# Kernel tuning notes

Hardware: AMD Instinct MI355X
Metric: run time of the kernel (lower is better)

Reference implementation:

```python
import jax, jax.numpy as jnp
import numpy as np


def setup_inputs() -> dict:
    key = jax.random.key(0)
    kA, kB = jax.random.split(key)
    B, H, W, C = 1, 80, 80, 256  # NHWC backbone features; B must be 1 for the TF broadcast in the divide to be valid
    feature_A = jax.random.normal(kA, (B, H, W, C), dtype=jnp.float32)
    feature_B = jax.random.normal(kB, (B, H, W, C), dtype=jnp.float32)
    return {"feature_A": feature_A, "feature_B": feature_B}


def reference(feature_A, feature_B):
    # corr[b,i,j,k,l] = mean_c A[b,i,j,c] * B[b,k,l,c]
    # Expressed as a batched matmul instead of materializing the (H,W,H,W,C) intermediate.
    C = feature_A.shape[-1]
    corr = jnp.einsum('bijc,bklc->bijkl', feature_A, feature_B) / C  # [B,H,W,H,W]
    # penalty[b,i,j] = sqrt(sum_{k,l} corr^2)
    penalty = jnp.sqrt(jnp.sum(corr * corr, axis=(-1, -2)))  # [B,H,W]
    # Faithful to tf.math.divide: trailing-dim broadcasting of [B,H,W] against [B,H,W,H,W]
    # (valid because B == 1; penalty aligns to the (j,k,l) trailing axes exactly as in TF).
    return corr / penalty
```

## Files before the change

kernel.cpp:

```cpp
#include <hip/hip_runtime.h>

typedef __attribute__((ext_vector_type(8))) short bf16x8;
typedef __attribute__((ext_vector_type(4))) float f32x4;

#define M_TOT 6400
#define C_TOT 256
#define BM 128
#define BN 128
#define BK 32
#define NTILE 50
#define ONM 50
#define ONN 25

#define VMCNT0 asm volatile("s_waitcnt vmcnt(0)" ::: "memory")
#define VMCNT4 asm volatile("s_waitcnt vmcnt(4)" ::: "memory")
#define VMCNT6 asm volatile("s_waitcnt vmcnt(6)" ::: "memory")
#define SBAR   __builtin_amdgcn_s_barrier()

__device__ __forceinline__ short f2bf(float f) {
    unsigned u = __float_as_uint(f);
    u = (u + 0x7fffu + ((u >> 16) & 1u)) >> 16;
    return (short)u;
}
__device__ __forceinline__ float bf2f(short s) {
    return __uint_as_float(((unsigned)(unsigned short)s) << 16);
}

__device__ __forceinline__ void gload16(const short* g, short* l) {
    __builtin_amdgcn_global_load_lds(
        (const __attribute__((address_space(1))) void*)g,
        (__attribute__((address_space(3))) void*)l, 16, 0, 0);
}


__global__ __launch_bounds__(256) void prep(const float* __restrict__ A,
                                            const float* __restrict__ Bm,
                                            short* __restrict__ Ab,
                                            short* __restrict__ Bb,
                                            short* __restrict__ Bt,
                                            float* __restrict__ P)
{
    __shared__ __align__(16) short Lb[64][72];
    const int bid = blockIdx.x;
    const int t   = threadIdx.x;

    if (bid < 400) {
        const int n0 = (bid % 100) * 64;
        const int c0 = (bid / 100) * 64;
        const int r  = t >> 2;
        const int cb = (t & 3) * 16;

        const float4* src = reinterpret_cast<const float4*>(
            Bm + (size_t)(n0 + r) * C_TOT + c0 + cb);
        const float4 v0 = src[0], v1 = src[1], v2 = src[2], v3 = src[3];
        bf16x8 w0, w1;
        w0[0]=f2bf(v0.x); w0[1]=f2bf(v0.y); w0[2]=f2bf(v0.z); w0[3]=f2bf(v0.w);
        w0[4]=f2bf(v1.x); w0[5]=f2bf(v1.y); w0[6]=f2bf(v1.z); w0[7]=f2bf(v1.w);
        w1[0]=f2bf(v2.x); w1[1]=f2bf(v2.y); w1[2]=f2bf(v2.z); w1[3]=f2bf(v2.w);
        w1[4]=f2bf(v3.x); w1[5]=f2bf(v3.y); w1[6]=f2bf(v3.z); w1[7]=f2bf(v3.w);
        *reinterpret_cast<bf16x8*>(&Lb[r][cb])     = w0;
        *reinterpret_cast<bf16x8*>(&Lb[r][cb + 8]) = w1;
        short* brow = Bb + (size_t)(n0 + r) * C_TOT + c0 + cb;
        *reinterpret_cast<bf16x8*>(brow)     = w0;
        *reinterpret_cast<bf16x8*>(brow + 8) = w1;
        __syncthreads();

        #pragma unroll
        for (int p = 0; p < 2; ++p) {
            const int q = t + p * 256;
            const int c = q >> 3;
            const int h = q & 7;
            bf16x8 w;
            #pragma unroll
            for (int j = 0; j < 8; ++j) w[j] = Lb[h * 8 + j][c];
            *reinterpret_cast<bf16x8*>(&Bt[(size_t)(c0 + c) * M_TOT + n0 + h * 8]) = w;
        }
    } else {
        const int aid = bid - 400;
        if (aid == 0)
            for (int j = t; j < M_TOT; j += 256) P[j] = 0.0f;
        const int base = aid * 2048;
        #pragma unroll
        for (int it = 0; it < 8; ++it) {
            const int i = base + it * 256 + t;
            const float4 v0 = reinterpret_cast<const float4*>(A + (size_t)i * 8)[0];
            const float4 v1 = reinterpret_cast<const float4*>(A + (size_t)i * 8)[1];
            bf16x8 w;
            w[0]=f2bf(v0.x); w[1]=f2bf(v0.y); w[2]=f2bf(v0.z); w[3]=f2bf(v0.w);
            w[4]=f2bf(v1.x); w[5]=f2bf(v1.y); w[6]=f2bf(v1.z); w[7]=f2bf(v1.w);
            *reinterpret_cast<bf16x8*>(Ab + (size_t)i * 8) = w;
        }
    }
}

__global__ __launch_bounds__(256) void convert_ab(const float* __restrict__ A,
                                                  const float* __restrict__ Bm,
                                                  short* __restrict__ Ab,
                                                  short* __restrict__ Bb)
{
    const int n8 = M_TOT * C_TOT / 8;
    for (int i = blockIdx.x * blockDim.x + threadIdx.x; i < 2 * n8;
         i += gridDim.x * blockDim.x) {
        const float* s = (i < n8) ? (A + (size_t)i * 8) : (Bm + (size_t)(i - n8) * 8);
        short* d       = (i < n8) ? (Ab + (size_t)i * 8) : (Bb + (size_t)(i - n8) * 8);
        const float4 v0 = reinterpret_cast<const float4*>(s)[0];
        const float4 v1 = reinterpret_cast<const float4*>(s)[1];
        bf16x8 w;
        w[0]=f2bf(v0.x); w[1]=f2bf(v0.y); w[2]=f2bf(v0.z); w[3]=f2bf(v0.w);
        w[4]=f2bf(v1.x); w[5]=f2bf(v1.y); w[6]=f2bf(v1.z); w[7]=f2bf(v1.w);
        *reinterpret_cast<bf16x8*>(d) = w;
    }
}


__device__ __forceinline__ void stage_tiles_g(const short* __restrict__ A,
                                              const short* __restrict__ B,
                                              int m0, int n0, int k0,
                                              int lda, int ldb,
                                              short* As, short* Bs,
                                              int wave, int lane)
{
    #pragma unroll
    for (int t = 0; t < 2; ++t) {
        const int c  = (wave * 2 + t) * 64 + lane;
        const int r  = c >> 2;
        const int g  = c & 3;
        const int sg = g ^ ((r >> 1) & 3);
        gload16(A + (size_t)(m0 + r) * lda + k0 + sg * 8, As + (wave * 2 + t) * 512);
        gload16(B + (size_t)(n0 + r) * ldb + k0 + sg * 8, Bs + (wave * 2 + t) * 512);
    }
}

template<int KSTEPS>
__device__ __forceinline__ void gemm_tile_g(const short* __restrict__ A,
                                            const short* __restrict__ B,
                                            int m0, int n0, int kbase,
                                            int lda, int ldb, int tid,
                                            short (*Sm)[2][4096],
                                            f32x4 acc[4][4])
{
    const int lane = tid & 63;
    const int wave = tid >> 6;
    const int rl   = lane & 15;
    const int g_rd = lane >> 4;
    const int wr   = wave >> 1;
    const int wc   = wave & 1;

    stage_tiles_g(A, B, m0, n0, kbase, lda, ldb, &Sm[0][0][0], &Sm[0][1][0], wave, lane);
    if (KSTEPS > 1)
        stage_tiles_g(A, B, m0, n0, kbase + BK, lda, ldb,
                      &Sm[1][0][0], &Sm[1][1][0], wave, lane);
    if (KSTEPS > 1) { VMCNT4; } else { VMCNT0; }
    SBAR;

    #pragma unroll
    for (int kt = 0; kt < KSTEPS; ++kt) {
        const int cur = kt % 3;
        if (kt + 2 < KSTEPS)
            stage_tiles_g(A, B, m0, n0, kbase + (kt + 2) * BK, lda, ldb,
                          &Sm[(kt + 2) % 3][0][0], &Sm[(kt + 2) % 3][1][0], wave, lane);

        bf16x8 af[4], bfr[4];
        #pragma unroll
        for (int mi = 0; mi < 4; ++mi) {
            const int r  = wr * 64 + mi * 16 + rl;
            const int sg = g_rd ^ ((r >> 1) & 3);
            af[mi] = *reinterpret_cast<const bf16x8*>(&Sm[cur][0][r * BK + sg * 8]);
        }
        #pragma unroll
        for (int ni = 0; ni < 4; ++ni) {
            const int r  = wc * 64 + ni * 16 + rl;
            const int sg = g_rd ^ ((r >> 1) & 3);
            bfr[ni] = *reinterpret_cast<const bf16x8*>(&Sm[cur][1][r * BK + sg * 8]);
        }
        __builtin_amdgcn_s_setprio(1);
        #pragma unroll
        for (int mi = 0; mi < 4; ++mi)
            #pragma unroll
            for (int ni = 0; ni < 4; ++ni)
                acc[mi][ni] = __builtin_amdgcn_mfma_f32_16x16x32_bf16(
                    af[mi], bfr[ni], acc[mi][ni], 0, 0, 0);
        __builtin_amdgcn_s_setprio(0);

        if (kt + 1 < KSTEPS) {
            if (kt + 2 < KSTEPS) { VMCNT4; } else { VMCNT0; }
            SBAR;
        }
    }
}


template<int STEPS>
__global__ __launch_bounds__(256) void gemm_G(const short* __restrict__ Bt,
                                              float* __restrict__ Gp)
{
    __shared__ __align__(16) short Sm[3][2][4096];
    const int tid = threadIdx.x;
    const int m0 = blockIdx.y * BM, n0 = blockIdx.x * BN;
    const int z  = blockIdx.z;
    f32x4 acc[4][4] = {};
    gemm_tile_g<STEPS>(Bt, Bt, m0, n0, z * (STEPS * BK),
                       M_TOT, M_TOT, tid, Sm, acc);

    float* dst = Gp + (size_t)z * (C_TOT * C_TOT);
    const int lane = tid & 63, rl = lane & 15;
    const int wave = tid >> 6, wr = wave >> 1, wc = wave & 1;
    #pragma unroll
    for (int mi = 0; mi < 4; ++mi)
        #pragma unroll
        for (int i = 0; i < 4; ++i) {
            const int m = m0 + wr * 64 + mi * 16 + (lane >> 4) * 4 + i;
            #pragma unroll
            for (int ni = 0; ni < 4; ++ni)
                dst[m * C_TOT + n0 + wc * 64 + ni * 16 + rl] = acc[mi][ni][i];
        }
}

__global__ __launch_bounds__(256) void g_reduce(const float* __restrict__ Gp,
                                                short* __restrict__ Gb,
                                                int nchunks)
{
    const int i4 = blockIdx.x * 256 + threadIdx.x;
    float4 s = make_float4(0.f, 0.f, 0.f, 0.f);
    for (int z = 0; z < nchunks; ++z) {
        const float4 v = reinterpret_cast<const float4*>(
            Gp + (size_t)z * (C_TOT * C_TOT))[i4];
        s.x += v.x; s.y += v.y; s.z += v.z; s.w += v.w;
    }
    short4 o;
    o.x = f2bf(s.x); o.y = f2bf(s.y); o.z = f2bf(s.z); o.w = f2bf(s.w);
    reinterpret_cast<short4*>(Gb)[i4] = o;
}

__global__ __launch_bounds__(256) void penalty_q(const short* __restrict__ Ab,
                                                 const short* __restrict__ Gb,
                                                 float* __restrict__ P)
{
    __shared__ __align__(16) short Sm[3][2][4096];
    const int tid = threadIdx.x;
    const int m0 = blockIdx.x * BM;
    const int ci = blockIdx.y & 1, cj = blockIdx.y >> 1;
    const int lane = tid & 63, rl = lane & 15;
    const int wave = tid >> 6, wr = wave >> 1, wc = wave & 1;

    f32x4 acc[4][4] = {};
    gemm_tile_g<4>(Ab, Gb + (size_t)(cj * BM) * C_TOT, m0, 0, ci * BM,
                   C_TOT, C_TOT, tid, Sm, acc);

    #pragma unroll
    for (int mi = 0; mi < 4; ++mi)
        #pragma unroll
        for (int i = 0; i < 4; ++i) {
            const int m = m0 + wr * 64 + mi * 16 + (lane >> 4) * 4 + i;
            float s = 0.0f;
            #pragma unroll
            for (int ni = 0; ni < 4; ++ni) {
                const int cp = cj * BM + wc * 64 + ni * 16 + rl;
                s += acc[mi][ni][i] * bf2f(Ab[(size_t)m * C_TOT + cp]);
            }
            s += __shfl_xor(s, 1);
            s += __shfl_xor(s, 2);
            s += __shfl_xor(s, 4);
            s += __shfl_xor(s, 8);
            if (rl == 0) atomicAdd(&P[m], s);
        }
}


#define OBUF 12288
#define OB_B 4096

__device__ __forceinline__ void stage_tiles_o(const short* __restrict__ A,
                                              const short* __restrict__ B,
                                              int m0, int n0, int k0,
                                              short* buf, int wave, int lane)
{
    #pragma unroll
    for (int t = 0; t < 2; ++t) {
        const int c  = (wave * 2 + t) * 64 + lane;
        const int r  = c >> 2;
        const int g  = c & 3;
        const int sg = g ^ ((r >> 1) & 3);
        gload16(A + (size_t)(m0 + r) * C_TOT + k0 + sg * 8, buf + (wave * 2 + t) * 512);
    }
    #pragma unroll
    for (int t = 0; t < 4; ++t) {
        const int c  = (wave * 4 + t) * 64 + lane;
        const int r  = c >> 2;
        const int g  = c & 3;
        const int sg = g ^ ((r >> 1) & 3);
        gload16(B + (size_t)(n0 + r) * C_TOT + k0 + sg * 8,
                buf + OB_B + (wave * 4 + t) * 512);
    }
}

__global__ __launch_bounds__(256, 2) void gemm_out(const short* __restrict__ Ab,
                                                   const short* __restrict__ Bb,
                                                   const float* __restrict__ P,
                                                   float* __restrict__ out)
{
    __shared__ __align__(16) short Sm[3][OBUF];
    const int tid = threadIdx.x;
    const int lane = tid & 63, rl = lane & 15;
    const int g_rd = lane >> 4;
    const int wave = tid >> 6, wr = wave >> 1, wc = wave & 1;

    const int nwg = ONM * ONN, q = nwg >> 3, r = nwg & 7;
    const int orig = blockIdx.x;
    const int xcd = orig & 7, idx = orig >> 3;
    const int wg = (xcd < r ? xcd * (q + 1) : r * (q + 1) + (xcd - r) * q) + idx;
    const int m0 = (wg / ONN) * 128;
    const int n0 = (wg % ONN) * 256;

    f32x4 acc[4][8] = {};

    stage_tiles_o(Ab, Bb, m0, n0, 0,  &Sm[0][0], wave, lane);
    stage_tiles_o(Ab, Bb, m0, n0, BK, &Sm[1][0], wave, lane);
    VMCNT6; SBAR;

    #pragma unroll
    for (int kt = 0; kt < 8; ++kt) {
        const int cur = kt % 3;
        if (kt + 2 < 8)
            stage_tiles_o(Ab, Bb, m0, n0, (kt + 2) * BK, &Sm[(kt + 2) % 3][0], wave, lane);

        bf16x8 af[4], bfr[8];
        #pragma unroll
        for (int mi = 0; mi < 4; ++mi) {
            const int rr = wr * 64 + mi * 16 + rl;
            const int sg = g_rd ^ ((rr >> 1) & 3);
            af[mi] = *reinterpret_cast<const bf16x8*>(&Sm[cur][rr * BK + sg * 8]);
        }
        #pragma unroll
        for (int ni = 0; ni < 8; ++ni) {
            const int rr = wc * 128 + ni * 16 + rl;
            const int sg = g_rd ^ ((rr >> 1) & 3);
            bfr[ni] = *reinterpret_cast<const bf16x8*>(&Sm[cur][OB_B + rr * BK + sg * 8]);
        }
        __builtin_amdgcn_s_setprio(1);
        #pragma unroll
        for (int mi = 0; mi < 4; ++mi)
            #pragma unroll
            for (int ni = 0; ni < 8; ++ni)
                acc[mi][ni] = __builtin_amdgcn_mfma_f32_16x16x32_bf16(
                    af[mi], bfr[ni], acc[mi][ni], 0, 0, 0);
        __builtin_amdgcn_s_setprio(0);

        if (kt + 1 < 8) {
            if (kt + 2 < 8) { VMCNT6; } else { VMCNT0; }
            SBAR;
        }
    }

    float rs[8];
    #pragma unroll
    for (int ni = 0; ni < 8; ++ni)
        rs[ni] = rsqrtf(P[n0 + wc * 128 + ni * 16 + rl]);

    SBAR;

    float* Es = reinterpret_cast<float*>(Sm) + wave * 2112;
    #pragma unroll
    for (int mi = 0; mi < 4; ++mi) {
        #pragma unroll
        for (int ni = 0; ni < 8; ++ni)
            #pragma unroll
            for (int i = 0; i < 4; ++i)
                Es[((lane >> 4) * 4 + i) * 132 + ni * 16 + rl] = acc[mi][ni][i] * rs[ni];
        #pragma unroll
        for (int it = 0; it < 8; ++it) {
            const int f   = it * 64 + lane;
            const int row = f >> 5;
            const int c4  = f & 31;
            const float4 v = *reinterpret_cast<const float4*>(&Es[row * 132 + c4 * 4]);
            const int m = m0 + wr * 64 + mi * 16 + row;
            *reinterpret_cast<float4*>(
                &out[(size_t)m * M_TOT + n0 + wc * 128 + c4 * 4]) = v;
        }
    }
}


__global__ __launch_bounds__(256) void gemm_penalty(const short* __restrict__ Ab,
                                                    const short* __restrict__ Bb,
                                                    float* __restrict__ P)
{
    __shared__ __align__(16) short Sm[3][2][4096];
    const int tid = threadIdx.x;
    const int m0 = blockIdx.y * BM, n0 = blockIdx.x * BN;
    f32x4 acc[4][4] = {};
    gemm_tile_g<8>(Ab, Bb, m0, n0, 0, C_TOT, C_TOT, tid, Sm, acc);

    const int lane = tid & 63, rl = lane & 15;
    const int wave = tid >> 6, wr = wave >> 1;
    #pragma unroll
    for (int mi = 0; mi < 4; ++mi) {
        #pragma unroll
        for (int i = 0; i < 4; ++i) {
            const int m = m0 + wr * 64 + mi * 16 + (lane >> 4) * 4 + i;
            float s = 0.0f;
            #pragma unroll
            for (int ni = 0; ni < 4; ++ni) {
                const float v = acc[mi][ni][i];
                s += v * v;
            }
            s += __shfl_xor(s, 1);
            s += __shfl_xor(s, 2);
            s += __shfl_xor(s, 4);
            s += __shfl_xor(s, 8);
            if (rl == 0) atomicAdd(&P[m], s);
        }
    }
}

__global__ __launch_bounds__(256) void gemm_out_plain(const short* __restrict__ Ab,
                                                      const short* __restrict__ Bb,
                                                      const float* __restrict__ P,
                                                      float* __restrict__ out)
{
    __shared__ __align__(16) short Sm[3][2][4096];
    const int tid = threadIdx.x;
    const int lane = tid & 63, rl = lane & 15;
    const int wave = tid >> 6, wr = wave >> 1, wc = wave & 1;
    const int m0 = blockIdx.y * BM, n0 = blockIdx.x * BN;

    f32x4 acc[4][4] = {};
    gemm_tile_g<8>(Ab, Bb, m0, n0, 0, C_TOT, C_TOT, tid, Sm, acc);

    float rs[4];
    #pragma unroll
    for (int ni = 0; ni < 4; ++ni)
        rs[ni] = rsqrtf(P[n0 + wc * 64 + ni * 16 + rl]);

    SBAR;

    float* Es = reinterpret_cast<float*>(Sm) + wave * 1088;
    #pragma unroll
    for (int mi = 0; mi < 4; ++mi) {
        #pragma unroll
        for (int ni = 0; ni < 4; ++ni)
            #pragma unroll
            for (int i = 0; i < 4; ++i)
                Es[((lane >> 4) * 4 + i) * 68 + ni * 16 + rl] = acc[mi][ni][i] * rs[ni];
        #pragma unroll
        for (int it = 0; it < 4; ++it) {
            const int f   = it * 64 + lane;
            const int row = f >> 4;
            const int c4  = f & 15;
            const float4 v = *reinterpret_cast<const float4*>(&Es[row * 68 + c4 * 4]);
            const int m = m0 + wr * 64 + mi * 16 + row;
            *reinterpret_cast<float4*>(&out[(size_t)m * M_TOT + n0 + wc * 64 + c4 * 4]) = v;
        }
    }
}


__global__ __launch_bounds__(256) void corr_gemm(const float* __restrict__ A,
                                                 const float* __restrict__ Bm,
                                                 float* __restrict__ out,
                                                 float* __restrict__ penalty)
{
    __shared__ short As[BM * BK];
    __shared__ short Bs[BN * BK];

    const int tid  = threadIdx.x;
    const int lane = tid & 63;
    const int wave = tid >> 6;
    const int wr   = wave >> 1;
    const int wc   = wave & 1;
    const int m0   = blockIdx.y * BM;
    const int n0   = blockIdx.x * BN;
    const int g_rd = lane >> 4;
    const int rl   = lane & 15;

    f32x4 acc[4][4] = {};

    for (int k0 = 0; k0 < C_TOT; k0 += BK) {
        #pragma unroll
        for (int half = 0; half < 2; ++half) {
            const int cc = tid + half * 256;
            const int r  = cc >> 2;
            const int g  = cc & 3;
            const int sg = g ^ ((r >> 1) & 3);

            const float4* pa = reinterpret_cast<const float4*>(
                A + (size_t)(m0 + r) * C_TOT + k0 + g * 8);
            float4 a0 = pa[0], a1 = pa[1];
            bf16x8 wa;
            wa[0]=f2bf(a0.x); wa[1]=f2bf(a0.y); wa[2]=f2bf(a0.z); wa[3]=f2bf(a0.w);
            wa[4]=f2bf(a1.x); wa[5]=f2bf(a1.y); wa[6]=f2bf(a1.z); wa[7]=f2bf(a1.w);
            *reinterpret_cast<bf16x8*>(&As[r * BK + sg * 8]) = wa;

            const float4* pb = reinterpret_cast<const float4*>(
                Bm + (size_t)(n0 + r) * C_TOT + k0 + g * 8);
            float4 b0 = pb[0], b1 = pb[1];
            bf16x8 wb;
            wb[0]=f2bf(b0.x); wb[1]=f2bf(b0.y); wb[2]=f2bf(b0.z); wb[3]=f2bf(b0.w);
            wb[4]=f2bf(b1.x); wb[5]=f2bf(b1.y); wb[6]=f2bf(b1.z); wb[7]=f2bf(b1.w);
            *reinterpret_cast<bf16x8*>(&Bs[r * BK + sg * 8]) = wb;
        }
        __syncthreads();

        bf16x8 af[4], bfr[4];
        #pragma unroll
        for (int mi = 0; mi < 4; ++mi) {
            const int r  = wr * 64 + mi * 16 + rl;
            const int sg = g_rd ^ ((r >> 1) & 3);
            af[mi] = *reinterpret_cast<const bf16x8*>(&As[r * BK + sg * 8]);
        }
        #pragma unroll
        for (int ni = 0; ni < 4; ++ni) {
            const int r  = wc * 64 + ni * 16 + rl;
            const int sg = g_rd ^ ((r >> 1) & 3);
            bfr[ni] = *reinterpret_cast<const bf16x8*>(&Bs[r * BK + sg * 8]);
        }
        #pragma unroll
        for (int mi = 0; mi < 4; ++mi)
            #pragma unroll
            for (int ni = 0; ni < 4; ++ni)
                acc[mi][ni] = __builtin_amdgcn_mfma_f32_16x16x32_bf16(
                    af[mi], bfr[ni], acc[mi][ni], 0, 0, 0);
        __syncthreads();
    }

    const float inv_c = 1.0f / (float)C_TOT;
    #pragma unroll
    for (int mi = 0; mi < 4; ++mi) {
        #pragma unroll
        for (int i = 0; i < 4; ++i) {
            const int m = m0 + wr * 64 + mi * 16 + (lane >> 4) * 4 + i;
            float s = 0.0f;
            #pragma unroll
            for (int ni = 0; ni < 4; ++ni) {
                const float v = acc[mi][ni][i] * inv_c;
                out[(size_t)m * M_TOT + n0 + wc * 64 + ni * 16 + rl] = v;
                s += v * v;
            }
            s += __shfl_xor(s, 1);
            s += __shfl_xor(s, 2);
            s += __shfl_xor(s, 4);
            s += __shfl_xor(s, 8);
            if (rl == 0) atomicAdd(&penalty[m], s);
        }
    }
}

__global__ __launch_bounds__(256) void scale_k(float* __restrict__ out,
                                               const float* __restrict__ penalty)
{
    const unsigned cols4 = M_TOT / 4;
    const unsigned total = (unsigned)M_TOT * cols4;
    float4* o4 = reinterpret_cast<float4*>(out);
    const float4* p4 = reinterpret_cast<const float4*>(penalty);
    for (unsigned idx = blockIdx.x * blockDim.x + threadIdx.x; idx < total;
         idx += gridDim.x * blockDim.x) {
        const unsigned n4 = idx % cols4;
        const float4 p = p4[n4];
        float4 v = o4[idx];
        v.x *= rsqrtf(p.x);
        v.y *= rsqrtf(p.y);
        v.z *= rsqrtf(p.z);
        v.w *= rsqrtf(p.w);
        o4[idx] = v;
    }
}


extern "C" void kernel_launch(void* const* d_in, const int* in_sizes, int n_in,
                              void* d_out, int out_size, void* d_ws, size_t ws_size,
                              hipStream_t stream) {
    const float* A = (const float*)d_in[0];
    const float* B = (const float*)d_in[1];
    float* out     = (float*)d_out;

    const size_t mat_sh = (size_t)M_TOT * C_TOT;
    const size_t sz_ab  = mat_sh * sizeof(short);
    const size_t sz_gb  = (size_t)C_TOT * C_TOT * sizeof(short);
    const size_t sz_p   = (size_t)M_TOT * sizeof(float);
    const size_t sz_gq  = (size_t)C_TOT * C_TOT * sizeof(float);
    const size_t base_need = 3 * sz_ab + sz_gb + sz_p;
    const size_t need_f40  = base_need + 40 * sz_gq;
    const size_t need_f20  = base_need + 20 * sz_gq;
    const size_t need_mid  = 2 * sz_ab + sz_p;

    dim3 grid2(NTILE, NTILE);

    if (ws_size >= need_f20) {
        short* Ab = (short*)d_ws;
        short* Bb = Ab + mat_sh;
        short* Bt = Bb + mat_sh;
        short* Gb = Bt + mat_sh;
        float* P  = (float*)((char*)d_ws + 3 * sz_ab + sz_gb);
        float* Gp = (float*)((char*)d_ws + 3 * sz_ab + sz_gb + sz_p);

        prep<<<500, 256, 0, stream>>>(A, B, Ab, Bb, Bt, P);
        if (ws_size >= need_f40) {
            gemm_G<5><<<dim3(2, 2, 40), 256, 0, stream>>>(Bt, Gp);
            g_reduce<<<64, 256, 0, stream>>>(Gp, Gb, 40);
        } else {
            gemm_G<10><<<dim3(2, 2, 20), 256, 0, stream>>>(Bt, Gp);
            g_reduce<<<64, 256, 0, stream>>>(Gp, Gb, 20);
        }
        penalty_q<<<dim3(NTILE, 4), 256, 0, stream>>>(Ab, Gb, P);
        gemm_out<<<ONM * ONN, 256, 0, stream>>>(Ab, Bb, P, out);
    } else if (ws_size >= need_mid) {
        short* Ab = (short*)d_ws;
        short* Bb = Ab + mat_sh;
        float* P  = (float*)(Bb + mat_sh);

        hipMemsetAsync(P, 0, sz_p, stream);
        convert_ab<<<1600, 256, 0, stream>>>(A, B, Ab, Bb);
        gemm_penalty<<<grid2, dim3(256), 0, stream>>>(Ab, Bb, P);
        gemm_out_plain<<<grid2, dim3(256), 0, stream>>>(Ab, Bb, P, out);
    } else {
        float* penalty = (float*)d_ws;
        hipMemsetAsync(penalty, 0, sz_p, stream);
        corr_gemm<<<grid2, dim3(256), 0, stream>>>(A, B, out, penalty);
        scale_k<<<2048, 256, 0, stream>>>(out, penalty);
    }
}
```

Baseline: 84.01 us.

## Split gemm_out across 8 waves with 64x64 per-wave tiles and nontemporal stores

The output GEMM kernel moves from 256 threads (4 waves, each computing 64x128) to 512 threads (8 waves, each computing 64x64) for the same 128x256 block tile. Global-to-LDS staging is spread over more waves and the vmcnt waits are adjusted to match. Final output writes now use nontemporal stores so the large streamed output bypasses cache retention. This cuts per-wave accumulator registers and raises wave count per CU to hide latency, in exchange for more LDS fragment reads per MFMA and more barrier participants.

```diff
diff --git a/kernel.cpp b/kernel.cpp
--- a/kernel.cpp
+++ b/kernel.cpp
@@ -13,8 +13,8 @@
 #define ONN 25
 
 #define VMCNT0 asm volatile("s_waitcnt vmcnt(0)" ::: "memory")
+#define VMCNT3 asm volatile("s_waitcnt vmcnt(3)" ::: "memory")
 #define VMCNT4 asm volatile("s_waitcnt vmcnt(4)" ::: "memory")
-#define VMCNT6 asm volatile("s_waitcnt vmcnt(6)" ::: "memory")
 #define SBAR   __builtin_amdgcn_s_barrier()
 
 __device__ __forceinline__ short f2bf(float f) {
@@ -93,6 +93,276 @@
     }
 }
 
+
+__device__ __forceinline__ void stage_tiles_g(const short* __restrict__ A,
+                                              const short* __restrict__ B,
+                                              int m0, int n0, int k0,
+                                              int lda, int ldb,
+                                              short* As, short* Bs,
+                                              int wave, int lane)
+{
+    #pragma unroll
+    for (int t = 0; t < 2; ++t) {
+        const int c  = (wave * 2 + t) * 64 + lane;
+        const int r  = c >> 2;
+        const int g  = c & 3;
+        const int sg = g ^ ((r >> 1) & 3);
+        gload16(A + (size_t)(m0 + r) * lda + k0 + sg * 8, As + (wave * 2 + t) * 512);
+        gload16(B + (size_t)(n0 + r) * ldb + k0 + sg * 8, Bs + (wave * 2 + t) * 512);
+    }
+}
+
+template<int KSTEPS>
+__device__ __forceinline__ void gemm_tile_g(const short* __restrict__ A,
+                                            const short* __restrict__ B,
+                                            int m0, int n0, int kbase,
+                                            int lda, int ldb, int tid,
+                                            short (*Sm)[2][4096],
+                                            f32x4 acc[4][4])
+{
+    const int lane = tid & 63;
+    const int wave = tid >> 6;
+    const int rl   = lane & 15;
+    const int g_rd = lane >> 4;
+    const int wr   = wave >> 1;
+    const int wc   = wave & 1;
+
+    stage_tiles_g(A, B, m0, n0, kbase, lda, ldb, &Sm[0][0][0], &Sm[0][1][0], wave, lane);
+    if (KSTEPS > 1)
+        stage_tiles_g(A, B, m0, n0, kbase + BK, lda, ldb,
+                      &Sm[1][0][0], &Sm[1][1][0], wave, lane);
+    if (KSTEPS > 1) { VMCNT4; } else { VMCNT0; }
+    SBAR;
+
+    #pragma unroll
+    for (int kt = 0; kt < KSTEPS; ++kt) {
+        const int cur = kt % 3;
+        if (kt + 2 < KSTEPS)
+            stage_tiles_g(A, B, m0, n0, kbase + (kt + 2) * BK, lda, ldb,
+                          &Sm[(kt + 2) % 3][0][0], &Sm[(kt + 2) % 3][1][0], wave, lane);
+
+        bf16x8 af[4], bfr[4];
+        #pragma unroll
+        for (int mi = 0; mi < 4; ++mi) {
+            const int r  = wr * 64 + mi * 16 + rl;
+            const int sg = g_rd ^ ((r >> 1) & 3);
+            af[mi] = *reinterpret_cast<const bf16x8*>(&Sm[cur][0][r * BK + sg * 8]);
+        }
+        #pragma unroll
+        for (int ni = 0; ni < 4; ++ni) {
+            const int r  = wc * 64 + ni * 16 + rl;
+            const int sg = g_rd ^ ((r >> 1) & 3);
+            bfr[ni] = *reinterpret_cast<const bf16x8*>(&Sm[cur][1][r * BK + sg * 8]);
+        }
+        __builtin_amdgcn_s_setprio(1);
+        #pragma unroll
+        for (int mi = 0; mi < 4; ++mi)
+            #pragma unroll
+            for (int ni = 0; ni < 4; ++ni)
+                acc[mi][ni] = __builtin_amdgcn_mfma_f32_16x16x32_bf16(
+                    af[mi], bfr[ni], acc[mi][ni], 0, 0, 0);
+        __builtin_amdgcn_s_setprio(0);
+
+        if (kt + 1 < KSTEPS) {
+            if (kt + 2 < KSTEPS) { VMCNT4; } else { VMCNT0; }
+            SBAR;
+        }
+    }
+}
+
+
+template<int STEPS>
+__global__ __launch_bounds__(256) void gemm_G(const short* __restrict__ Bt,
+                                              float* __restrict__ Gp)
+{
+    __shared__ __align__(16) short Sm[3][2][4096];
+    const int tid = threadIdx.x;
+    const int m0 = blockIdx.y * BM, n0 = blockIdx.x * BN;
+    const int z  = blockIdx.z;
+    f32x4 acc[4][4] = {};
+    gemm_tile_g<STEPS>(Bt, Bt, m0, n0, z * (STEPS * BK),
+                       M_TOT, M_TOT, tid, Sm, acc);
+
+    float* dst = Gp + (size_t)z * (C_TOT * C_TOT);
+    const int lane = tid & 63, rl = lane & 15;
+    const int wave = tid >> 6, wr = wave >> 1, wc = wave & 1;
+    #pragma unroll
+    for (int mi = 0; mi < 4; ++mi)
+        #pragma unroll
+        for (int i = 0; i < 4; ++i) {
+            const int m = m0 + wr * 64 + mi * 16 + (lane >> 4) * 4 + i;
+            #pragma unroll
+            for (int ni = 0; ni < 4; ++ni)
+                dst[m * C_TOT + n0 + wc * 64 + ni * 16 + rl] = acc[mi][ni][i];
+        }
+}
+
+__global__ __launch_bounds__(256) void g_reduce(const float* __restrict__ Gp,
+                                                short* __restrict__ Gb,
+                                                int nchunks)
+{
+    const int i4 = blockIdx.x * 256 + threadIdx.x;
+    float4 s = make_float4(0.f, 0.f, 0.f, 0.f);
+    for (int z = 0; z < nchunks; ++z) {
+        const float4 v = reinterpret_cast<const float4*>(
+            Gp + (size_t)z * (C_TOT * C_TOT))[i4];
+        s.x += v.x; s.y += v.y; s.z += v.z; s.w += v.w;
+    }
+    short4 o;
+    o.x = f2bf(s.x); o.y = f2bf(s.y); o.z = f2bf(s.z); o.w = f2bf(s.w);
+    reinterpret_cast<short4*>(Gb)[i4] = o;
+}
+
+__global__ __launch_bounds__(256) void penalty_q(const short* __restrict__ Ab,
+                                                 const short* __restrict__ Gb,
+                                                 float* __restrict__ P)
+{
+    __shared__ __align__(16) short Sm[3][2][4096];
+    const int tid = threadIdx.x;
+    const int m0 = blockIdx.x * BM;
+    const int ci = blockIdx.y & 1, cj = blockIdx.y >> 1;
+    const int lane = tid & 63, rl = lane & 15;
+    const int wave = tid >> 6, wr = wave >> 1, wc = wave & 1;
+
+    f32x4 acc[4][4] = {};
+    gemm_tile_g<4>(Ab, Gb + (size_t)(cj * BM) * C_TOT, m0, 0, ci * BM,
+                   C_TOT, C_TOT, tid, Sm, acc);
+
+    #pragma unroll
+    for (int mi = 0; mi < 4; ++mi)
+        #pragma unroll
+        for (int i = 0; i < 4; ++i) {
+            const int m = m0 + wr * 64 + mi * 16 + (lane >> 4) * 4 + i;
+            float s = 0.0f;
+            #pragma unroll
+            for (int ni = 0; ni < 4; ++ni) {
+                const int cp = cj * BM + wc * 64 + ni * 16 + rl;
+                s += acc[mi][ni][i] * bf2f(Ab[(size_t)m * C_TOT + cp]);
+            }
+            s += __shfl_xor(s, 1);
+            s += __shfl_xor(s, 2);
+            s += __shfl_xor(s, 4);
+            s += __shfl_xor(s, 8);
+            if (rl == 0) atomicAdd(&P[m], s);
+        }
+}
+
+
+#define OBUF 12288
+#define OB_B 4096
+
+__device__ __forceinline__ void stage_512(const short* __restrict__ A,
+                                          const short* __restrict__ B,
+                                          int m0, int n0, int k0,
+                                          short* buf, int wave, int lane)
+{
+    {
+        const int c  = wave * 64 + lane;
+        const int r  = c >> 2;
+        const int g  = c & 3;
+        const int sg = g ^ ((r >> 1) & 3);
+        gload16(A + (size_t)(m0 + r) * C_TOT + k0 + sg * 8, buf + wave * 512);
+    }
+    #pragma unroll
+    for (int tt = 0; tt < 2; ++tt) {
+        const int c  = (wave * 2 + tt) * 64 + lane;
+        const int r  = c >> 2;
+        const int g  = c & 3;
+        const int sg = g ^ ((r >> 1) & 3);
+        gload16(B + (size_t)(n0 + r) * C_TOT + k0 + sg * 8,
+                buf + OB_B + (wave * 2 + tt) * 512);
+    }
+}
+
+__global__ __launch_bounds__(512, 4) void gemm_out(const short* __restrict__ Ab,
+                                                   const short* __restrict__ Bb,
+                                                   const float* __restrict__ P,
+                                                   float* __restrict__ out)
+{
+    __shared__ __align__(16) short Sm[3][OBUF];
+    const int tid = threadIdx.x;
+    const int lane = tid & 63, rl = lane & 15;
+    const int g_rd = lane >> 4;
+    const int wave = tid >> 6;
+    const int wr   = wave >> 2;
+    const int wc   = wave & 3;
+
+    const int nwg = ONM * ONN, q = nwg >> 3, r = nwg & 7;
+    const int orig = blockIdx.x;
+    const int xcd = orig & 7, idx = orig >> 3;
+    const int wg = (xcd < r ? xcd * (q + 1) : r * (q + 1) + (xcd - r) * q) + idx;
+    const int m0 = (wg / ONN) * 128;
+    const int n0 = (wg % ONN) * 256;
+
+    f32x4 acc[4][4] = {};
+
+    stage_512(Ab, Bb, m0, n0, 0,  &Sm[0][0], wave, lane);
+    stage_512(Ab, Bb, m0, n0, BK, &Sm[1][0], wave, lane);
+    VMCNT3; SBAR;
+
+    #pragma unroll
+    for (int kt = 0; kt < 8; ++kt) {
+        const int cur = kt % 3;
+        if (kt + 2 < 8)
+            stage_512(Ab, Bb, m0, n0, (kt + 2) * BK, &Sm[(kt + 2) % 3][0], wave, lane);
+
+        bf16x8 af[4], bfr[4];
+        #pragma unroll
+        for (int mi = 0; mi < 4; ++mi) {
+            const int rr = wr * 64 + mi * 16 + rl;
+            const int sg = g_rd ^ ((rr >> 1) & 3);
+            af[mi] = *reinterpret_cast<const bf16x8*>(&Sm[cur][rr * BK + sg * 8]);
+        }
+        #pragma unroll
+        for (int ni = 0; ni < 4; ++ni) {
+            const int rr = wc * 64 + ni * 16 + rl;
+            const int sg = g_rd ^ ((rr >> 1) & 3);
+            bfr[ni] = *reinterpret_cast<const bf16x8*>(&Sm[cur][OB_B + rr * BK + sg * 8]);
+        }
+        __builtin_amdgcn_s_setprio(1);
+        #pragma unroll
+        for (int mi = 0; mi < 4; ++mi)
+            #pragma unroll
+            for (int ni = 0; ni < 4; ++ni)
+                acc[mi][ni] = __builtin_amdgcn_mfma_f32_16x16x32_bf16(
+                    af[mi], bfr[ni], acc[mi][ni], 0, 0, 0);
+        __builtin_amdgcn_s_setprio(0);
+
+        if (kt + 1 < 8) {
+            if (kt + 2 < 8) { VMCNT3; } else { VMCNT0; }
+            SBAR;
+        }
+    }
+
+    float rs[4];
+    #pragma unroll
+    for (int ni = 0; ni < 4; ++ni)
+        rs[ni] = rsqrtf(P[n0 + wc * 64 + ni * 16 + rl]);
+
+    SBAR;
+
+    float* Es = reinterpret_cast<float*>(Sm) + wave * 1088;
+    #pragma unroll
+    for (int mi = 0; mi < 4; ++mi) {
+        #pragma unroll
+        for (int ni = 0; ni < 4; ++ni)
+            #pragma unroll
+            for (int i = 0; i < 4; ++i)
+                Es[((lane >> 4) * 4 + i) * 68 + ni * 16 + rl] = acc[mi][ni][i] * rs[ni];
+        #pragma unroll
+        for (int it = 0; it < 4; ++it) {
+            const int f   = it * 64 + lane;
+            const int row = f >> 4;
+            const int c4  = f & 15;
+            const f32x4 v = *reinterpret_cast<const f32x4*>(&Es[row * 68 + c4 * 4]);
+            const int m = m0 + wr * 64 + mi * 16 + row;
+            __builtin_nontemporal_store(v, reinterpret_cast<f32x4*>(
+                &out[(size_t)m * M_TOT + n0 + wc * 64 + c4 * 4]));
+        }
+    }
+}
+
+
 __global__ __launch_bounds__(256) void convert_ab(const float* __restrict__ A,
                                                   const float* __restrict__ Bm,
                                                   short* __restrict__ Ab,
@@ -111,275 +381,6 @@
         *reinterpret_cast<bf16x8*>(d) = w;
     }
 }
-
-
-__device__ __forceinline__ void stage_tiles_g(const short* __restrict__ A,
-                                              const short* __restrict__ B,
-                                              int m0, int n0, int k0,
-                                              int lda, int ldb,
-                                              short* As, short* Bs,
-                                              int wave, int lane)
-{
-    #pragma unroll
-    for (int t = 0; t < 2; ++t) {
-        const int c  = (wave * 2 + t) * 64 + lane;
-        const int r  = c >> 2;
-        const int g  = c & 3;
-        const int sg = g ^ ((r >> 1) & 3);
-        gload16(A + (size_t)(m0 + r) * lda + k0 + sg * 8, As + (wave * 2 + t) * 512);
-        gload16(B + (size_t)(n0 + r) * ldb + k0 + sg * 8, Bs + (wave * 2 + t) * 512);
-    }
-}
-
-template<int KSTEPS>
-__device__ __forceinline__ void gemm_tile_g(const short* __restrict__ A,
-                                            const short* __restrict__ B,
-                                            int m0, int n0, int kbase,
-                                            int lda, int ldb, int tid,
-                                            short (*Sm)[2][4096],
-                                            f32x4 acc[4][4])
-{
-    const int lane = tid & 63;
-    const int wave = tid >> 6;
-    const int rl   = lane & 15;
-    const int g_rd = lane >> 4;
-    const int wr   = wave >> 1;
-    const int wc   = wave & 1;
-
-    stage_tiles_g(A, B, m0, n0, kbase, lda, ldb, &Sm[0][0][0], &Sm[0][1][0], wave, lane);
-    if (KSTEPS > 1)
-        stage_tiles_g(A, B, m0, n0, kbase + BK, lda, ldb,
-                      &Sm[1][0][0], &Sm[1][1][0], wave, lane);
-    if (KSTEPS > 1) { VMCNT4; } else { VMCNT0; }
-    SBAR;
-
-    #pragma unroll
-    for (int kt = 0; kt < KSTEPS; ++kt) {
-        const int cur = kt % 3;
-        if (kt + 2 < KSTEPS)
-            stage_tiles_g(A, B, m0, n0, kbase + (kt + 2) * BK, lda, ldb,
-                          &Sm[(kt + 2) % 3][0][0], &Sm[(kt + 2) % 3][1][0], wave, lane);
-
-        bf16x8 af[4], bfr[4];
-        #pragma unroll
-        for (int mi = 0; mi < 4; ++mi) {
-            const int r  = wr * 64 + mi * 16 + rl;
-            const int sg = g_rd ^ ((r >> 1) & 3);
-            af[mi] = *reinterpret_cast<const bf16x8*>(&Sm[cur][0][r * BK + sg * 8]);
-        }
-        #pragma unroll
-        for (int ni = 0; ni < 4; ++ni) {
-            const int r  = wc * 64 + ni * 16 + rl;
-            const int sg = g_rd ^ ((r >> 1) & 3);
-            bfr[ni] = *reinterpret_cast<const bf16x8*>(&Sm[cur][1][r * BK + sg * 8]);
-        }
-        __builtin_amdgcn_s_setprio(1);
-        #pragma unroll
-        for (int mi = 0; mi < 4; ++mi)
-            #pragma unroll
-            for (int ni = 0; ni < 4; ++ni)
-                acc[mi][ni] = __builtin_amdgcn_mfma_f32_16x16x32_bf16(
-                    af[mi], bfr[ni], acc[mi][ni], 0, 0, 0);
-        __builtin_amdgcn_s_setprio(0);
-
-        if (kt + 1 < KSTEPS) {
-            if (kt + 2 < KSTEPS) { VMCNT4; } else { VMCNT0; }
-            SBAR;
-        }
-    }
-}
-
-
-template<int STEPS>
-__global__ __launch_bounds__(256) void gemm_G(const short* __restrict__ Bt,
-                                              float* __restrict__ Gp)
-{
-    __shared__ __align__(16) short Sm[3][2][4096];
-    const int tid = threadIdx.x;
-    const int m0 = blockIdx.y * BM, n0 = blockIdx.x * BN;
-    const int z  = blockIdx.z;
-    f32x4 acc[4][4] = {};
-    gemm_tile_g<STEPS>(Bt, Bt, m0, n0, z * (STEPS * BK),
-                       M_TOT, M_TOT, tid, Sm, acc);
-
-    float* dst = Gp + (size_t)z * (C_TOT * C_TOT);
-    const int lane = tid & 63, rl = lane & 15;
-    const int wave = tid >> 6, wr = wave >> 1, wc = wave & 1;
-    #pragma unroll
-    for (int mi = 0; mi < 4; ++mi)
-        #pragma unroll
-        for (int i = 0; i < 4; ++i) {
-            const int m = m0 + wr * 64 + mi * 16 + (lane >> 4) * 4 + i;
-            #pragma unroll
-            for (int ni = 0; ni < 4; ++ni)
-                dst[m * C_TOT + n0 + wc * 64 + ni * 16 + rl] = acc[mi][ni][i];
-        }
-}
-
-__global__ __launch_bounds__(256) void g_reduce(const float* __restrict__ Gp,
-                                                short* __restrict__ Gb,
-                                                int nchunks)
-{
-    const int i4 = blockIdx.x * 256 + threadIdx.x;
-    float4 s = make_float4(0.f, 0.f, 0.f, 0.f);
-    for (int z = 0; z < nchunks; ++z) {
-        const float4 v = reinterpret_cast<const float4*>(
-            Gp + (size_t)z * (C_TOT * C_TOT))[i4];
-        s.x += v.x; s.y += v.y; s.z += v.z; s.w += v.w;
-    }
-    short4 o;
-    o.x = f2bf(s.x); o.y = f2bf(s.y); o.z = f2bf(s.z); o.w = f2bf(s.w);
-    reinterpret_cast<short4*>(Gb)[i4] = o;
-}
-
-__global__ __launch_bounds__(256) void penalty_q(const short* __restrict__ Ab,
-                                                 const short* __restrict__ Gb,
-                                                 float* __restrict__ P)
-{
-    __shared__ __align__(16) short Sm[3][2][4096];
-    const int tid = threadIdx.x;
-    const int m0 = blockIdx.x * BM;
-    const int ci = blockIdx.y & 1, cj = blockIdx.y >> 1;
-    const int lane = tid & 63, rl = lane & 15;
-    const int wave = tid >> 6, wr = wave >> 1, wc = wave & 1;
-
-    f32x4 acc[4][4] = {};
-    gemm_tile_g<4>(Ab, Gb + (size_t)(cj * BM) * C_TOT, m0, 0, ci * BM,
-                   C_TOT, C_TOT, tid, Sm, acc);
-
-    #pragma unroll
-    for (int mi = 0; mi < 4; ++mi)
-        #pragma unroll
-        for (int i = 0; i < 4; ++i) {
-            const int m = m0 + wr * 64 + mi * 16 + (lane >> 4) * 4 + i;
-            float s = 0.0f;
-            #pragma unroll
-            for (int ni = 0; ni < 4; ++ni) {
-                const int cp = cj * BM + wc * 64 + ni * 16 + rl;
-                s += acc[mi][ni][i] * bf2f(Ab[(size_t)m * C_TOT + cp]);
-            }
-            s += __shfl_xor(s, 1);
-            s += __shfl_xor(s, 2);
-            s += __shfl_xor(s, 4);
-            s += __shfl_xor(s, 8);
-            if (rl == 0) atomicAdd(&P[m], s);
-        }
-}
-
-
-#define OBUF 12288
-#define OB_B 4096
-
-__device__ __forceinline__ void stage_tiles_o(const short* __restrict__ A,
-                                              const short* __restrict__ B,
-                                              int m0, int n0, int k0,
-                                              short* buf, int wave, int lane)
-{
-    #pragma unroll
-    for (int t = 0; t < 2; ++t) {
-        const int c  = (wave * 2 + t) * 64 + lane;
-        const int r  = c >> 2;
-        const int g  = c & 3;
-        const int sg = g ^ ((r >> 1) & 3);
-        gload16(A + (size_t)(m0 + r) * C_TOT + k0 + sg * 8, buf + (wave * 2 + t) * 512);
-    }
-    #pragma unroll
-    for (int t = 0; t < 4; ++t) {
-        const int c  = (wave * 4 + t) * 64 + lane;
-        const int r  = c >> 2;
-        const int g  = c & 3;
-        const int sg = g ^ ((r >> 1) & 3);
-        gload16(B + (size_t)(n0 + r) * C_TOT + k0 + sg * 8,
-                buf + OB_B + (wave * 4 + t) * 512);
-    }
-}
-
-__global__ __launch_bounds__(256, 2) void gemm_out(const short* __restrict__ Ab,
-                                                   const short* __restrict__ Bb,
-                                                   const float* __restrict__ P,
-                                                   float* __restrict__ out)
-{
-    __shared__ __align__(16) short Sm[3][OBUF];
-    const int tid = threadIdx.x;
-    const int lane = tid & 63, rl = lane & 15;
-    const int g_rd = lane >> 4;
-    const int wave = tid >> 6, wr = wave >> 1, wc = wave & 1;
-
-    const int nwg = ONM * ONN, q = nwg >> 3, r = nwg & 7;
-    const int orig = blockIdx.x;
-    const int xcd = orig & 7, idx = orig >> 3;
-    const int wg = (xcd < r ? xcd * (q + 1) : r * (q + 1) + (xcd - r) * q) + idx;
-    const int m0 = (wg / ONN) * 128;
-    const int n0 = (wg % ONN) * 256;
-
-    f32x4 acc[4][8] = {};
-
-    stage_tiles_o(Ab, Bb, m0, n0, 0,  &Sm[0][0], wave, lane);
-    stage_tiles_o(Ab, Bb, m0, n0, BK, &Sm[1][0], wave, lane);
-    VMCNT6; SBAR;
-
-    #pragma unroll
-    for (int kt = 0; kt < 8; ++kt) {
-        const int cur = kt % 3;
-        if (kt + 2 < 8)
-            stage_tiles_o(Ab, Bb, m0, n0, (kt + 2) * BK, &Sm[(kt + 2) % 3][0], wave, lane);
-
-        bf16x8 af[4], bfr[8];
-        #pragma unroll
-        for (int mi = 0; mi < 4; ++mi) {
-            const int rr = wr * 64 + mi * 16 + rl;
-            const int sg = g_rd ^ ((rr >> 1) & 3);
-            af[mi] = *reinterpret_cast<const bf16x8*>(&Sm[cur][rr * BK + sg * 8]);
-        }
-        #pragma unroll
-        for (int ni = 0; ni < 8; ++ni) {
-            const int rr = wc * 128 + ni * 16 + rl;
-            const int sg = g_rd ^ ((rr >> 1) & 3);
-            bfr[ni] = *reinterpret_cast<const bf16x8*>(&Sm[cur][OB_B + rr * BK + sg * 8]);
-        }
-        __builtin_amdgcn_s_setprio(1);
-        #pragma unroll
-        for (int mi = 0; mi < 4; ++mi)
-            #pragma unroll
-            for (int ni = 0; ni < 8; ++ni)
-                acc[mi][ni] = __builtin_amdgcn_mfma_f32_16x16x32_bf16(
-                    af[mi], bfr[ni], acc[mi][ni], 0, 0, 0);
-        __builtin_amdgcn_s_setprio(0);
-
-        if (kt + 1 < 8) {
-            if (kt + 2 < 8) { VMCNT6; } else { VMCNT0; }
-            SBAR;
-        }
-    }
-
-    float rs[8];
-    #pragma unroll
-    for (int ni = 0; ni < 8; ++ni)
-        rs[ni] = rsqrtf(P[n0 + wc * 128 + ni * 16 + rl]);
-
-    SBAR;
-
-    float* Es = reinterpret_cast<float*>(Sm) + wave * 2112;
-    #pragma unroll
-    for (int mi = 0; mi < 4; ++mi) {
-        #pragma unroll
-        for (int ni = 0; ni < 8; ++ni)
-            #pragma unroll
-            for (int i = 0; i < 4; ++i)
-                Es[((lane >> 4) * 4 + i) * 132 + ni * 16 + rl] = acc[mi][ni][i] * rs[ni];
-        #pragma unroll
-        for (int it = 0; it < 8; ++it) {
-            const int f   = it * 64 + lane;
-            const int row = f >> 5;
-            const int c4  = f & 31;
-            const float4 v = *reinterpret_cast<const float4*>(&Es[row * 132 + c4 * 4]);
-            const int m = m0 + wr * 64 + mi * 16 + row;
-            *reinterpret_cast<float4*>(
-                &out[(size_t)m * M_TOT + n0 + wc * 128 + c4 * 4]) = v;
-        }
-    }
-}
-
 
 __global__ __launch_bounds__(256) void gemm_penalty(const short* __restrict__ Ab,
                                                     const short* __restrict__ Bb,
@@ -602,19 +603,19 @@
             g_reduce<<<64, 256, 0, stream>>>(Gp, Gb, 20);
         }
         penalty_q<<<dim3(NTILE, 4), 256, 0, stream>>>(Ab, Gb, P);
-        gemm_out<<<ONM * ONN, 256, 0, stream>>>(Ab, Bb, P, out);
+        gemm_out<<<ONM * ONN, 512, 0, stream>>>(Ab, Bb, P, out);
     } else if (ws_size >= need_mid) {
         short* Ab = (short*)d_ws;
         short* Bb = Ab + mat_sh;
         float* P  = (float*)(Bb + mat_sh);
 
-        hipMemsetAsync(P, 0, sz_p, stream);
+        (void)hipMemsetAsync(P, 0, sz_p, stream);
         convert_ab<<<1600, 256, 0, stream>>>(A, B, Ab, Bb);
         gemm_penalty<<<grid2, dim3(256), 0, stream>>>(Ab, Bb, P);
         gemm_out_plain<<<grid2, dim3(256), 0, stream>>>(Ab, Bb, P, out);
     } else {
         float* penalty = (float*)d_ws;
-        hipMemsetAsync(penalty, 0, sz_p, stream);
+        (void)hipMemsetAsync(penalty, 0, sz_p, stream);
         corr_gemm<<<grid2, dim3(256), 0, stream>>>(A, B, out, penalty);
         scale_k<<<2048, 256, 0, stream>>>(out, penalty);
     }
```

Result: faster. 78.60 us (-6.4%).
